# Kernel tuning notes

Measured on AMD Instinct MI355X. Metric: run time of the kernel, lower is better.

The kernel has to match this reference:

```python
import jax, jax.numpy as jnp
import numpy as np

B, N, D = 4, 2048, 1024
WIN, K, ALPHA = 4, 8, 0.3


def setup_inputs() -> dict:
    key = jax.random.key(0)
    ks = jax.random.split(key, 16)
    s_d = 1.0 / np.sqrt(D)
    s_2d = 1.0 / np.sqrt(2 * D)
    inp = {
        'mu': jax.random.normal(ks[0], (B, N, D), jnp.float32),
        'pheromone': jax.random.uniform(ks[1], (B, N), jnp.float32),
        'Wq': jax.random.normal(ks[2], (D, D), jnp.float32) * s_d,
        'bq': jnp.zeros((D,), jnp.float32),
        'Wk': jax.random.normal(ks[3], (D, D), jnp.float32) * s_d,
        'bk': jnp.zeros((D,), jnp.float32),
        'Wv': jax.random.normal(ks[4], (D, D), jnp.float32) * s_d,
        'bv': jnp.zeros((D,), jnp.float32),
        'Wm1': jax.random.normal(ks[5], (2 * D, D), jnp.float32) * s_2d,
        'bm1': jnp.zeros((D,), jnp.float32),
        'Wm2': jax.random.normal(ks[6], (D, D), jnp.float32) * s_d,
        'bm2': jnp.zeros((D,), jnp.float32),
        'Wo': jax.random.normal(ks[7], (2 * D, D), jnp.float32) * s_2d,
        'bo': jnp.zeros((D,), jnp.float32),
    }
    return inp


def reference(mu, pheromone, Wq, bq, Wk, bk, Wv, bv, Wm1, bm1, Wm2, bm2, Wo, bo):
    # ---- local windowed gather-MLP ----
    padded = jnp.pad(mu, ((0, 0), (WIN, 0), (0, 0)))  # causal left-pad
    neighbors = jnp.stack([padded[:, WIN - w:WIN - w + N, :] for w in range(1, WIN + 1)], axis=2)
    self_exp = jnp.broadcast_to(mu[:, :, None, :], neighbors.shape)
    cat = jnp.concatenate([self_exp, neighbors], axis=-1)
    h = jax.nn.silu(cat @ Wm1 + bm1) @ Wm2 + bm2
    local_msgs = h.mean(axis=2)  # (B,N,D)

    # ---- causal top-k attention with pheromone bias ----
    q = mu @ Wq + bq
    k = mu @ Wk + bk
    v = mu @ Wv + bv
    scale = 1.0 / jnp.sqrt(jnp.asarray(D, mu.dtype))
    scores = jnp.einsum('bnd,bmd->bnm', q, k) * scale  # (B,N,N)
    scores = scores + ALPHA * pheromone[:, None, :]
    row = jnp.arange(N)
    causal = jnp.where(row[None, :] > row[:, None], -jnp.inf, 0.0).astype(mu.dtype)
    scores = scores + causal[None]
    # top-k sparsification (N > K): softmax over the k kept scores, zeros elsewhere
    vals, idx = jax.lax.top_k(scores, K)  # (B,N,K)
    probs = jax.nn.softmax(vals, axis=-1)
    bi = jnp.arange(B)[:, None, None]
    ni = jnp.arange(N)[None, :, None]
    attn = jnp.zeros_like(scores).at[bi, ni, idx].set(probs)
    global_msgs = jnp.einsum('bnm,bmd->bnd', attn, v)

    return jnp.concatenate([local_msgs, global_msgs], axis=-1) @ Wo + bo
```

## Files before the change

### kernel.cpp

```cpp
#include <hip/hip_runtime.h>
#include <hip/hip_bf16.h>
#include <math.h>

#define B_ 4
#define N_ 2048
#define D_ 1024
#define WIN_ 4
#define KTOP 8
#define ALPHA_ 0.3f
#define SCALE_ (1.0f/32.0f)
#define NCH 16
#define INV2048 0.00048828125f

typedef unsigned short ushortT;
typedef _Float16 halfT;
typedef __attribute__((ext_vector_type(8))) _Float16 half8v;
typedef __attribute__((ext_vector_type(4))) float f32x4;

__device__ inline ushortT h2u(halfT h){ union{halfT h; ushortT u;} x; x.h=h; return x.u; }
__device__ inline halfT  u2h(ushortT u){ union{halfT h; ushortT u;} x; x.u=u; return x.h; }
__device__ inline float  uh2f(ushortT u){ return (float)u2h(u); }

__device__ __forceinline__ void gll16(const ushortT* g, ushortT* l) {
    __builtin_amdgcn_global_load_lds(
        (const __attribute__((address_space(1))) void*)g,
        (__attribute__((address_space(3))) void*)l, 16, 0, 0);
}

__global__ __launch_bounds__(256)
void prep_all(const float* __restrict__ mu, const float* __restrict__ Wm1,
              const float* __restrict__ Wm2, const float* __restrict__ Wv,
              const float* __restrict__ Wo, const float* __restrict__ Wq,
              const float* __restrict__ Wk,
              ushortT* __restrict__ mu_a, ushortT* __restrict__ mu_B,
              ushortT* __restrict__ WtF, ushortT* __restrict__ Wt_m2,
              ushortT* __restrict__ Wt_v, ushortT* __restrict__ Wt_o,
              ushortT* __restrict__ WqT_a, ushortT* __restrict__ WqT_B,
              ushortT* __restrict__ WkT_a, ushortT* __restrict__ WkT_B)
{
    const int bid = blockIdx.x;
    if (bid < 8192) {
        size_t base = ((size_t)bid * 256 + threadIdx.x) * 4;
        float4 v = *reinterpret_cast<const float4*>(&mu[base]);
        float vv[4] = {v.x, v.y, v.z, v.w};
        ushort4 pa, pb;
#pragma unroll
        for (int j = 0; j < 4; ++j) {
            float f = vv[j];
            halfT a = (halfT)f;  float r = f - (float)a;
            halfT b = (halfT)(r * 2048.0f);
            ((ushortT*)&pa)[j] = h2u(a); ((ushortT*)&pb)[j] = h2u(b);
        }
        *reinterpret_cast<ushort4*>(&mu_a[base]) = pa;
        *reinterpret_cast<ushort4*>(&mu_B[base]) = pb;
        return;
    }
    __shared__ float t[32][33];
    int b = bid - 8192;
    const float* W; ushortT* Pa; ushortT* Pb = nullptr;
    int K, lb, split = 0;
    if (b < 1024)      { W = Wm1;                       Pa = WtF;                     K = 1024; lb = b; }
    else if (b < 2048) { W = Wm1 + (size_t)1024 * 1024; Pa = WtF + (size_t)1024*1024; K = 1024; lb = b - 1024; }
    else if (b < 3072) { W = Wm2;  Pa = Wt_m2; K = 1024; lb = b - 2048; }
    else if (b < 4096) { W = Wv;   Pa = Wt_v;  K = 1024; lb = b - 3072; }
    else if (b < 6144) { W = Wo;   Pa = Wt_o;  K = 2048; lb = b - 4096; }
    else if (b < 7168) { W = Wq;   Pa = WqT_a; Pb = WqT_B; K = 1024; lb = b - 6144; split = 1; }
    else               { W = Wk;   Pa = WkT_a; Pb = WkT_B; K = 1024; lb = b - 7168; split = 1; }
    const int Nn = 1024;
    const int k0 = (K == 2048) ? (lb & 63) * 32 : (lb & 31) * 32;
    const int n0 = (K == 2048) ? (lb >> 6) * 32 : (lb >> 5) * 32;
    const int tx = threadIdx.x & 31, ty8 = threadIdx.x >> 5;
#pragma unroll
    for (int p = 0; p < 4; ++p) {
        int kk = p * 8 + ty8;
        t[kk][tx] = W[(size_t)(k0 + kk) * Nn + n0 + tx];
    }
    __syncthreads();
#pragma unroll
    for (int p = 0; p < 4; ++p) {
        int nn = p * 8 + ty8;
        float f = t[tx][nn];
        size_t o = (size_t)(n0 + nn) * K + k0 + tx;
        if (split) {
            halfT a = (halfT)f;  float r = f - (float)a;
            halfT bb = (halfT)(r * 2048.0f);
            Pa[o] = h2u(a); Pb[o] = h2u(bb);
        } else {
            Pa[o] = h2u((halfT)f);
        }
    }
}

__device__ __forceinline__ void gemm_core_h(
    const ushortT* __restrict__ A, int lda, const ushortT* __restrict__ Bt, int ldb,
    const float* __restrict__ bias, void* __restrict__ Cout, int ldc, int K,
    int m0, int n0, int outHalf, ushortT* AsL, ushortT* BsL)
{
    const int tid = threadIdx.x;
    const int w = tid >> 6, lane = tid & 63;
    const int wr = w >> 1, wc = w & 1;

    f32x4 acc[4][4];
#pragma unroll
    for (int mi = 0; mi < 4; ++mi)
#pragma unroll
        for (int ni = 0; ni < 4; ++ni) acc[mi][ni] = (f32x4){0.f, 0.f, 0.f, 0.f};

    for (int k0 = 0; k0 < K; k0 += 64) {
#pragma unroll
        for (int it = 0; it < 4; ++it) {
            int idx = tid + it * 256;
            int row = idx >> 3, c = idx & 7;
            int4 va = *reinterpret_cast<const int4*>(&A[(size_t)(m0 + row) * lda + k0 + c * 8]);
            *reinterpret_cast<int4*>(&AsL[row * 72 + c * 8]) = va;
            int4 vb = *reinterpret_cast<const int4*>(&Bt[(size_t)(n0 + row) * ldb + k0 + c * 8]);
            *reinterpret_cast<int4*>(&BsL[row * 72 + c * 8]) = vb;
        }
        __syncthreads();
#pragma unroll
        for (int kh = 0; kh < 2; ++kh) {
            const int ko = kh * 32 + (lane >> 4) * 8;
            const int rr = lane & 15;
            half8v af[4], bf[4];
#pragma unroll
            for (int mi = 0; mi < 4; ++mi)
                af[mi] = *reinterpret_cast<const half8v*>(&AsL[(wr * 64 + mi * 16 + rr) * 72 + ko]);
#pragma unroll
            for (int ni = 0; ni < 4; ++ni)
                bf[ni] = *reinterpret_cast<const half8v*>(&BsL[(wc * 64 + ni * 16 + rr) * 72 + ko]);
#pragma unroll
            for (int mi = 0; mi < 4; ++mi)
#pragma unroll
                for (int ni = 0; ni < 4; ++ni)
                    acc[mi][ni] = __builtin_amdgcn_mfma_f32_16x16x32_f16(
                        af[mi], bf[ni], acc[mi][ni], 0, 0, 0);
        }
        __syncthreads();
    }

    const int r4 = (lane >> 4) * 4, cl = lane & 15;
#pragma unroll
    for (int mi = 0; mi < 4; ++mi)
#pragma unroll
        for (int ni = 0; ni < 4; ++ni) {
            int row = m0 + wr * 64 + mi * 16 + r4;
            int col = n0 + wc * 64 + ni * 16 + cl;
            float bb = bias ? bias[col] : 0.f;
#pragma unroll
            for (int r = 0; r < 4; ++r) {
                float v = acc[mi][ni][r] + bb;
                if (outHalf)
                    ((ushortT*)Cout)[(size_t)(row + r) * ldc + col] = h2u((halfT)v);
                else
                    ((float*)Cout)[(size_t)(row + r) * ldc + col] = v;
            }
        }
}

template<int OUT_HALF>
__global__ __launch_bounds__(256)
void mfma_gemm_h(const ushortT* __restrict__ A, int lda,
                 const ushortT* __restrict__ Bt, int ldb,
                 const float* __restrict__ bias,
                 void* __restrict__ Cout, int ldc, int K)
{
    __shared__ ushortT AsL[128 * 72];
    __shared__ ushortT BsL[128 * 72];
    gemm_core_h(A, lda, Bt, ldb, bias, Cout, ldc, K,
                blockIdx.y * 128, blockIdx.x * 128, OUT_HALF, AsL, BsL);
}

__global__ __launch_bounds__(256)
void gemm_pf_v(const ushortT* __restrict__ mu_a,
               const ushortT* __restrict__ WtF, const ushortT* __restrict__ Wt_v,
               const float* __restrict__ bv,
               float* __restrict__ PF, ushortT* __restrict__ Vb16)
{
    __shared__ ushortT AsL[128 * 72];
    __shared__ ushortT BsL[128 * 72];
    const int bid = blockIdx.x;
    if (bid < 1024) {
        gemm_core_h(mu_a, D_, WtF, D_, (const float*)nullptr, (void*)PF, 2 * D_, D_,
                    (bid >> 4) * 128, (bid & 15) * 128, 0, AsL, BsL);
    } else {
        const int b2 = bid - 1024;
        gemm_core_h(mu_a, D_, Wt_v, D_, bv, (void*)Vb16, D_, D_,
                    (b2 >> 3) * 128, (b2 & 7) * 128, 1, AsL, BsL);
    }
}

__global__ __launch_bounds__(256)
void silu_mean(const float* __restrict__ P, const float* __restrict__ bm1,
               ushortT* __restrict__ Sb)
{
    size_t idx4 = (size_t)blockIdx.x * blockDim.x + threadIdx.x;
    size_t base = idx4 << 2;
    int row = (int)(base >> 10);
    int col = (int)(base & 1023);
    int n = row & (N_ - 1);
    float4 a = *reinterpret_cast<const float4*>(&P[(size_t)row * 2048 + col]);
    float4 bb = *reinterpret_cast<const float4*>(&bm1[col]);
    a.x += bb.x; a.y += bb.y; a.z += bb.z; a.w += bb.w;
    float sx = 0.f, sy = 0.f, sz = 0.f, sw = 0.f;
#pragma unroll
    for (int w = 1; w <= WIN_; ++w) {
        float xx = a.x, xy = a.y, xz = a.z, xw = a.w;
        if (n >= w) {
            const float4 nb = *reinterpret_cast<const float4*>(
                &P[(size_t)(row - w) * 2048 + 1024 + col]);
            xx += nb.x; xy += nb.y; xz += nb.z; xw += nb.w;
        }
        sx += xx / (1.f + __expf(-xx));
        sy += xy / (1.f + __expf(-xy));
        sz += xz / (1.f + __expf(-xz));
        sw += xw / (1.f + __expf(-xw));
    }
    ushort4 o = {h2u((halfT)(sx * 0.25f)), h2u((halfT)(sy * 0.25f)),
                 h2u((halfT)(sz * 0.25f)), h2u((halfT)(sw * 0.25f))};
    *reinterpret_cast<ushort4*>(&Sb[base]) = o;
}

__device__ inline void topk_insert(float (&tv)[KTOP], int (&ti)[KTOP], float s, int m)
{
    if ((s > tv[KTOP-1]) || (s == tv[KTOP-1] && m < ti[KTOP-1])) {
        float cs = s; int ci = m;
#pragma unroll
        for (int q = 0; q < KTOP; ++q) {
            bool beats = (cs > tv[q]) || (cs == tv[q] && ci < ti[q]);
            if (beats) { float t0 = tv[q]; int t1 = ti[q];
                         tv[q] = cs; ti[q] = ci; cs = t0; ci = t1; }
        }
    }
}

#define SPLIT3H_COMPUTE(Tb, wr, wc, lane, acc0, acc1)                           \
    {                                                                           \
        const int rr_ = (lane) & 15, q_ = (lane) >> 4;                          \
        const int Rb0_ = (wc) * 32 + rr_;                                       \
        const int Rb1_ = Rb0_ + 16;                                             \
        half8v ba0_ = *reinterpret_cast<const half8v*>(                         \
            &Tb[2 * 4096 + Rb0_ * 32 + ((q_ ^ ((Rb0_ >> 1) & 3)) << 3)]);       \
        half8v ba1_ = *reinterpret_cast<const half8v*>(                         \
            &Tb[2 * 4096 + Rb1_ * 32 + ((q_ ^ ((Rb1_ >> 1) & 3)) << 3)]);       \
        half8v bB0_ = *reinterpret_cast<const half8v*>(                         \
            &Tb[3 * 4096 + Rb0_ * 32 + ((q_ ^ ((Rb0_ >> 1) & 3)) << 3)]);       \
        half8v bB1_ = *reinterpret_cast<const half8v*>(                         \
            &Tb[3 * 4096 + Rb1_ * 32 + ((q_ ^ ((Rb1_ >> 1) & 3)) << 3)]);       \
        _Pragma("unroll")                                                       \
        for (int mi_ = 0; mi_ < 4; ++mi_) {                                     \
            const int Ra_ = (wr) * 64 + mi_ * 16 + rr_;                         \
            const int sw_ = (q_ ^ ((Ra_ >> 1) & 3)) << 3;                       \
            half8v aA_ = *reinterpret_cast<const half8v*>(&Tb[Ra_ * 32 + sw_]); \
            acc0[mi_][0] = __builtin_amdgcn_mfma_f32_16x16x32_f16(              \
                aA_, ba0_, acc0[mi_][0], 0, 0, 0);                              \
            acc0[mi_][1] = __builtin_amdgcn_mfma_f32_16x16x32_f16(              \
                aA_, ba1_, acc0[mi_][1], 0, 0, 0);                              \
            acc1[mi_][0] = __builtin_amdgcn_mfma_f32_16x16x32_f16(              \
                aA_, bB0_, acc1[mi_][0], 0, 0, 0);                              \
            acc1[mi_][1] = __builtin_amdgcn_mfma_f32_16x16x32_f16(              \
                aA_, bB1_, acc1[mi_][1], 0, 0, 0);                              \
        }                                                                       \
        _Pragma("unroll")                                                       \
        for (int mi_ = 0; mi_ < 4; ++mi_) {                                     \
            const int Ra_ = (wr) * 64 + mi_ * 16 + rr_;                         \
            const int sw_ = (q_ ^ ((Ra_ >> 1) & 3)) << 3;                       \
            half8v aB_ = *reinterpret_cast<const half8v*>(                      \
                &Tb[4096 + Ra_ * 32 + sw_]);                                    \
            acc1[mi_][0] = __builtin_amdgcn_mfma_f32_16x16x32_f16(              \
                aB_, ba0_, acc1[mi_][0], 0, 0, 0);                              \
            acc1[mi_][1] = __builtin_amdgcn_mfma_f32_16x16x32_f16(              \
                aB_, ba1_, acc1[mi_][1], 0, 0, 0);                              \
        }                                                                       \
    }

#define STAGE4(lb, koff)                                                        \
    {                                                                           \
        gll16(gp + goff + (koff), lb);                                          \
        gll16(gp + goff + (koff) + 16 * D_, (lb) + 512);                        \
        gll16(gp + goff + (koff) + 32 * D_, (lb) + 1024);                       \
        gll16(gp + goff + (koff) + 48 * D_, (lb) + 1536);                       \
    }

__global__ __launch_bounds__(512, 2)
void qk_proj(const ushortT* __restrict__ A0, const ushortT* __restrict__ A1,
             const ushortT* __restrict__ QWa, const ushortT* __restrict__ QWB,
             const ushortT* __restrict__ KWa, const ushortT* __restrict__ KWB,
             const float* __restrict__ bq, const float* __restrict__ bk,
             ushortT* __restrict__ Qa, ushortT* __restrict__ QB,
             ushortT* __restrict__ Ka, ushortT* __restrict__ KB)
{
    __shared__ ushortT TT[2][16384];

    const int half = blockIdx.x >> 9;
    int lin = blockIdx.x & 511;
    lin = (lin & 7) * 64 + (lin >> 3);
    const int m0 = (lin >> 3) * 128;
    const int n0 = (lin & 7) * 128;

    const ushortT* B0 = half ? KWa : QWa;
    const ushortT* B1 = half ? KWB : QWB;
    const float* bias = half ? bk : bq;
    ushortT* Pa = half ? Ka : Qa;
    ushortT* Pb = half ? KB : QB;

    const int tid = threadIdx.x;
    const int wid = tid >> 6, lane = tid & 63;
    const int wr = wid >> 2, wc = wid & 3;

    const int pl = wid >> 1;
    const int hb = (wid & 1) * 64;
    const ushortT* gp = (pl == 0) ? A0 : (pl == 1) ? A1 : (pl == 2) ? B0 : B1;
    const int rbase = (pl < 2 ? m0 : n0) + hb + (lane >> 2);
    const int cg8 = ((lane & 3) ^ ((lane >> 3) & 3)) << 3;
    const size_t goff = (size_t)rbase * D_ + cg8;
    ushortT* lb0 = &TT[0][pl * 4096 + hb * 32];
    ushortT* lb1 = &TT[1][pl * 4096 + hb * 32];

    f32x4 acc0[4][2], acc1[4][2];
#pragma unroll
    for (int mi = 0; mi < 4; ++mi) {
        acc0[mi][0] = (f32x4){0,0,0,0}; acc0[mi][1] = (f32x4){0,0,0,0};
        acc1[mi][0] = (f32x4){0,0,0,0}; acc1[mi][1] = (f32x4){0,0,0,0};
    }

    STAGE4(lb0, 0)
    __syncthreads();

    int cur = 0;
    for (int ks = 0; ks < 32; ++ks) {
        if (ks < 31) {
            ushortT* lb = cur ? lb0 : lb1;
            STAGE4(lb, (size_t)(ks + 1) * 32)
        }
        const ushortT* Tb = &TT[cur][0];
        __builtin_amdgcn_s_setprio(1);
        SPLIT3H_COMPUTE(Tb, wr, wc, lane, acc0, acc1)
        __builtin_amdgcn_s_setprio(0);
        __syncthreads();
        cur ^= 1;
    }

    const int r4 = (lane >> 4) * 4, cl = lane & 15;
#pragma unroll
    for (int mi = 0; mi < 4; ++mi)
#pragma unroll
        for (int ni = 0; ni < 2; ++ni) {
            int col = n0 + wc * 32 + ni * 16 + cl;
            float bb = bias[col];
#pragma unroll
            for (int r = 0; r < 4; ++r) {
                int row = m0 + wr * 64 + mi * 16 + r4 + r;
                float v = acc0[mi][ni][r] + INV2048 * acc1[mi][ni][r] + bb;
                halfT a = (halfT)v;  float r1 = v - (float)a;
                halfT b = (halfT)(r1 * 2048.0f);
                size_t o = (size_t)row * D_ + col;
                Pa[o] = h2u(a); Pb[o] = h2u(b);
            }
        }
}

__global__ __launch_bounds__(512, 2)
void attn_scores_h(const ushortT* __restrict__ Qa, const ushortT* __restrict__ QB,
                   const ushortT* __restrict__ Ka, const ushortT* __restrict__ KB,
                   const float* __restrict__ pher,
                   float* __restrict__ WV, int* __restrict__ WI)
{
    __shared__ ushortT TT[2][16384];
    __shared__ float Ps[128];
    __shared__ float PV[32 * 4 * 8];
    __shared__ int   PI[32 * 4 * 8];
    float* MV = reinterpret_cast<float*>(&TT[0][0]);
    int*   MI = reinterpret_cast<int*>((char*)&TT[0][0] + 16384);

    int lin = blockIdx.y * 136 + blockIdx.x;
    lin = (lin & 7) * 68 + (lin >> 3);
    const int b = lin / 136;
    const int xy = lin - b * 136;
    int g = 0;
    while ((g + 1) * (g + 2) / 2 <= xy) ++g;
    const int ch = xy - g * (g + 1) / 2;
    const int n0 = g * 128;
    const int m0 = ch * 128;
    const size_t bN = (size_t)b * N_;

    const int tid = threadIdx.x;
    const int wid = tid >> 6, lane = tid & 63;
    const int wr = wid >> 2, wc = wid & 3;

    if (tid < 128) Ps[tid] = pher[bN + m0 + tid];

    const int pl = wid >> 1;
    const int hb = (wid & 1) * 64;
    const ushortT* gp = (pl == 0) ? Qa : (pl == 1) ? QB : (pl == 2) ? Ka : KB;
    const size_t rbase = bN + (pl < 2 ? n0 : m0) + hb + (lane >> 2);
    const int cg8 = ((lane & 3) ^ ((lane >> 3) & 3)) << 3;
    const size_t goff = rbase * (size_t)D_ + cg8;
    ushortT* lb0 = &TT[0][pl * 4096 + hb * 32];
    ushortT* lb1 = &TT[1][pl * 4096 + hb * 32];

    f32x4 acc0[4][2], acc1[4][2];
#pragma unroll
    for (int mi = 0; mi < 4; ++mi) {
        acc0[mi][0] = (f32x4){0,0,0,0}; acc0[mi][1] = (f32x4){0,0,0,0};
        acc1[mi][0] = (f32x4){0,0,0,0}; acc1[mi][1] = (f32x4){0,0,0,0};
    }

    STAGE4(lb0, 0)
    __syncthreads();

    int cur = 0;
    for (int ks = 0; ks < 32; ++ks) {
        if (ks < 31) {
            ushortT* lb = cur ? lb0 : lb1;
            STAGE4(lb, (size_t)(ks + 1) * 32)
        }
        const ushortT* Tb = &TT[cur][0];
        __builtin_amdgcn_s_setprio(1);
        SPLIT3H_COMPUTE(Tb, wr, wc, lane, acc0, acc1)
        __builtin_amdgcn_s_setprio(0);
        __syncthreads();
        cur ^= 1;
    }

    const int r4 = (lane >> 4) * 4, cl = lane & 15;
    for (int p = 0; p < 4; ++p) {
        __syncthreads();
        if (wr == (p >> 1)) {
#pragma unroll
            for (int mi2 = 0; mi2 < 2; ++mi2) {
                const int mi = (p & 1) * 2 + mi2;
#pragma unroll
                for (int ni = 0; ni < 2; ++ni) {
                    int col = wc * 32 + ni * 16 + cl;
                    int m = m0 + col;
#pragma unroll
                    for (int r = 0; r < 4; ++r) {
                        int rloc = mi2 * 16 + r4 + r;
                        int n = n0 + p * 32 + rloc;
                        bool ok = (m <= n);
                        float sc = acc0[mi][ni][r] + INV2048 * acc1[mi][ni][r];
                        MV[rloc * 128 + col] = ok ? (sc * SCALE_ + ALPHA_ * Ps[col])
                                                  : -INFINITY;
                        MI[rloc * 128 + col] = ok ? m : 0x7fffffff;
                    }
                }
            }
        }
        __syncthreads();
        if (tid < 128) {
            const int row = tid >> 2, q4 = tid & 3;
            float tv[KTOP]; int ti[KTOP];
#pragma unroll
            for (int j = 0; j < KTOP; ++j) { tv[j] = -INFINITY; ti[j] = 0x7fffffff; }
            for (int j = 0; j < 32; ++j) {
                float s2 = MV[row * 128 + q4 * 32 + j];
                if (s2 == -INFINITY) continue;
                topk_insert(tv, ti, s2, MI[row * 128 + q4 * 32 + j]);
            }
#pragma unroll
            for (int j = 0; j < KTOP; ++j) {
                PV[(row * 4 + q4) * 8 + j] = tv[j];
                PI[(row * 4 + q4) * 8 + j] = ti[j];
            }
        }
        __syncthreads();
        if (tid < 32) {
            float tv[KTOP]; int ti[KTOP];
#pragma unroll
            for (int j = 0; j < KTOP; ++j) { tv[j] = -INFINITY; ti[j] = 0x7fffffff; }
            for (int i = 0; i < 32; ++i) {
                float s2 = PV[tid * 32 + i];
                if (s2 == -INFINITY) continue;
                topk_insert(tv, ti, s2, PI[tid * 32 + i]);
            }
            int n = n0 + p * 32 + tid;
            size_t base = ((bN + n) * NCH + ch) * 8;
#pragma unroll
            for (int j = 0; j < KTOP; ++j) { WV[base + j] = tv[j]; WI[base + j] = ti[j]; }
        }
    }
}

__global__ __launch_bounds__(256)
void attn_merge(const float* __restrict__ WV, const int* __restrict__ WI,
                const ushortT* __restrict__ V, ushortT* __restrict__ CCb)
{
    __shared__ float CV[4][128];
    __shared__ int   CI[4][128];
    __shared__ float Pp[4][KTOP];
    __shared__ int   Pi[4][KTOP];

    const int tid  = threadIdx.x;
    const int wv   = tid >> 6;
    const int lane = tid & 63;
    const int rid  = blockIdx.x * 4 + wv;
    const int b    = rid >> 11;
    const int n    = rid & (N_ - 1);
    const int ncand = ((n >> 7) + 1) * 8;
    const size_t cbase = (size_t)rid * (NCH * 8);

#pragma unroll
    for (int t = 0; t < 2; ++t) {
        int i = lane + t * 64;
        if (i < ncand) { CV[wv][i] = WV[cbase + i]; CI[wv][i] = WI[cbase + i]; }
        else           { CV[wv][i] = -INFINITY;     CI[wv][i] = 0x7fffffff;   }
    }
    __syncthreads();

    if (lane == 0) {
        float tv[KTOP]; int ti[KTOP];
#pragma unroll
        for (int j = 0; j < KTOP; ++j) { tv[j] = -INFINITY; ti[j] = 0x7fffffff; }
        for (int i = 0; i < 128; ++i) {
            float s = CV[wv][i];
            if (s == -INFINITY) continue;
            topk_insert(tv, ti, s, CI[wv][i]);
        }
        float mx = tv[0];
        float e[KTOP]; float sum = 0.f;
#pragma unroll
        for (int j = 0; j < KTOP; ++j) {
            e[j] = (tv[j] == -INFINITY) ? 0.f : __expf(tv[j] - mx);
            sum += e[j];
        }
        float inv = 1.f / sum;
#pragma unroll
        for (int j = 0; j < KTOP; ++j) {
            Pp[wv][j] = e[j] * inv;
            Pi[wv][j] = (tv[j] == -INFINITY) ? 0 : ti[j];
        }
    }
    __syncthreads();

    const size_t vbase = (size_t)b * N_ * D_;
#pragma unroll
    for (int it = 0; it < 2; ++it) {
        int c8 = (it * 64 + lane) * 8;
        float o[8];
#pragma unroll
        for (int u = 0; u < 8; ++u) o[u] = 0.f;
#pragma unroll
        for (int j = 0; j < KTOP; ++j) {
            float p = Pp[wv][j];
            ushort4 v0 = *reinterpret_cast<const ushort4*>(
                &V[vbase + (size_t)Pi[wv][j] * D_ + c8]);
            ushort4 v1 = *reinterpret_cast<const ushort4*>(
                &V[vbase + (size_t)Pi[wv][j] * D_ + c8 + 4]);
            o[0] = fmaf(p, uh2f(v0.x), o[0]); o[1] = fmaf(p, uh2f(v0.y), o[1]);
            o[2] = fmaf(p, uh2f(v0.z), o[2]); o[3] = fmaf(p, uh2f(v0.w), o[3]);
            o[4] = fmaf(p, uh2f(v1.x), o[4]); o[5] = fmaf(p, uh2f(v1.y), o[5]);
            o[6] = fmaf(p, uh2f(v1.z), o[6]); o[7] = fmaf(p, uh2f(v1.w), o[7]);
        }
        ushort4 ob0 = {h2u((halfT)o[0]), h2u((halfT)o[1]), h2u((halfT)o[2]), h2u((halfT)o[3])};
        ushort4 ob1 = {h2u((halfT)o[4]), h2u((halfT)o[5]), h2u((halfT)o[6]), h2u((halfT)o[7])};
        *reinterpret_cast<ushort4*>(&CCb[(size_t)rid * 2048 + 1024 + c8]) = ob0;
        *reinterpret_cast<ushort4*>(&CCb[(size_t)rid * 2048 + 1024 + c8 + 4]) = ob1;
    }
}

extern "C" void kernel_launch(void* const* d_in, const int* in_sizes, int n_in,
                              void* d_out, int out_size, void* d_ws, size_t ws_size,
                              hipStream_t stream)
{
    const float* mu   = (const float*)d_in[0];
    const float* pher = (const float*)d_in[1];
    const float* Wq   = (const float*)d_in[2];
    const float* bq   = (const float*)d_in[3];
    const float* Wk   = (const float*)d_in[4];
    const float* bk   = (const float*)d_in[5];
    const float* Wv   = (const float*)d_in[6];
    const float* bv   = (const float*)d_in[7];
    const float* Wm1  = (const float*)d_in[8];
    const float* bm1  = (const float*)d_in[9];
    const float* Wm2  = (const float*)d_in[10];
    const float* bm2  = (const float*)d_in[11];
    const float* Wo   = (const float*)d_in[12];
    const float* bo   = (const float*)d_in[13];
    float* out = (float*)d_out;
    float* ws  = (float*)d_ws;

    const size_t SZ  = (size_t)B_ * N_ * D_;
    const size_t MEG = 1024 * 1024;
    const int M = B_ * N_;

    ushortT* CCb  = (ushortT*)ws;
    float*   PF   = ws + SZ;
    ushortT* Qa   = (ushortT*)(ws + SZ);
    ushortT* QB   = Qa + SZ;
    ushortT* Ka   = (ushortT*)(ws + 2 * SZ);
    ushortT* KB   = Ka + SZ;
    ushortT* mu_a = (ushortT*)(ws + 3 * SZ);
    ushortT* mu_B = mu_a + SZ;
    ushortT* Sb   = (ushortT*)(ws + 4 * SZ);
    float*   WVb  = (float*)(ws + 4 * SZ);
    int*     WIb  = (int*)(WVb + MEG);
    ushortT* Vb16 = (ushortT*)(ws + 4 * SZ + 4 * MEG);
    ushortT* U    = (ushortT*)(ws + 4 * SZ + 8 * MEG);
    ushortT* WtF  = U;
    ushortT* Wt_m2 = U + 2 * MEG;
    ushortT* Wt_v  = U + 3 * MEG;
    ushortT* WqT_a = U + 4 * MEG;        ushortT* WqT_B = U + 5 * MEG;
    ushortT* WkT_a = U + 6 * MEG;        ushortT* WkT_B = U + 7 * MEG;
    ushortT* Wt_o  = U + 8 * MEG;

    dim3 blk256(256), blk512(512);
    dim3 gD(8, 64);

    hipLaunchKernelGGL(prep_all, dim3(16384), blk256, 0, stream,
                       mu, Wm1, Wm2, Wv, Wo, Wq, Wk,
                       mu_a, mu_B, WtF, Wt_m2, Wt_v, Wt_o,
                       WqT_a, WqT_B, WkT_a, WkT_B);
    hipLaunchKernelGGL(gemm_pf_v, dim3(1536), blk256, 0, stream,
                       mu_a, WtF, Wt_v, bv, PF, Vb16);
    hipLaunchKernelGGL(silu_mean, dim3(SZ / 4 / 256), blk256, 0, stream, PF, bm1, Sb);
    hipLaunchKernelGGL((mfma_gemm_h<1>), gD, blk256, 0, stream,
                       Sb, D_, Wt_m2, D_, bm2, (void*)CCb, 2 * D_, D_);
    hipLaunchKernelGGL(qk_proj, dim3(1024), blk512, 0, stream,
                       mu_a, mu_B, WqT_a, WqT_B, WkT_a, WkT_B,
                       bq, bk, Qa, QB, Ka, KB);
    hipLaunchKernelGGL(attn_scores_h, dim3(136, B_), blk512, 0, stream,
                       Qa, QB, Ka, KB, pher, WVb, WIb);
    hipLaunchKernelGGL(attn_merge, dim3(M / 4), blk256, 0, stream, WVb, WIb, Vb16, CCb);
    hipLaunchKernelGGL((mfma_gemm_h<0>), gD, blk256, 0, stream,
                       CCb, 2 * D_, Wt_o, 2048, bo, (void*)out, D_, 2 * D_);

    (void)in_sizes; (void)n_in; (void)out_size; (void)ws_size;
}
```

Before: 739.3 us.

## Replace double-buffered LDS staging with single buffer in QK projection and scores

Removes the ping-pong LDS buffers in qk_proj and attn_scores_h, so each k-step loads its tile, syncs, computes, then syncs again. This halves the tile LDS footprint, which may let more blocks fit per CU. The cost is that global-to-LDS loads no longer overlap with MFMA compute and each iteration now waits on two barriers.

```diff
diff --git a/kernel.cpp b/kernel.cpp
--- a/kernel.cpp
+++ b/kernel.cpp
@@ -289,7 +289,7 @@
              ushortT* __restrict__ Qa, ushortT* __restrict__ QB,
              ushortT* __restrict__ Ka, ushortT* __restrict__ KB)
 {
-    __shared__ ushortT TT[2][16384];
+    __shared__ ushortT TT[16384];
 
     const int half = blockIdx.x >> 9;
     int lin = blockIdx.x & 511;
@@ -313,8 +313,7 @@
     const int rbase = (pl < 2 ? m0 : n0) + hb + (lane >> 2);
     const int cg8 = ((lane & 3) ^ ((lane >> 3) & 3)) << 3;
     const size_t goff = (size_t)rbase * D_ + cg8;
-    ushortT* lb0 = &TT[0][pl * 4096 + hb * 32];
-    ushortT* lb1 = &TT[1][pl * 4096 + hb * 32];
+    ushortT* lb0 = &TT[pl * 4096 + hb * 32];
 
     f32x4 acc0[4][2], acc1[4][2];
 #pragma unroll
@@ -323,21 +322,13 @@
         acc1[mi][0] = (f32x4){0,0,0,0}; acc1[mi][1] = (f32x4){0,0,0,0};
     }
 
-    STAGE4(lb0, 0)
-    __syncthreads();
-
-    int cur = 0;
     for (int ks = 0; ks < 32; ++ks) {
-        if (ks < 31) {
-            ushortT* lb = cur ? lb0 : lb1;
-            STAGE4(lb, (size_t)(ks + 1) * 32)
-        }
-        const ushortT* Tb = &TT[cur][0];
+        STAGE4(lb0, (size_t)ks * 32)
+        __syncthreads();
         __builtin_amdgcn_s_setprio(1);
-        SPLIT3H_COMPUTE(Tb, wr, wc, lane, acc0, acc1)
+        SPLIT3H_COMPUTE(TT, wr, wc, lane, acc0, acc1)
         __builtin_amdgcn_s_setprio(0);
         __syncthreads();
-        cur ^= 1;
     }
 
     const int r4 = (lane >> 4) * 4, cl = lane & 15;
@@ -365,12 +356,12 @@
                    const float* __restrict__ pher,
                    float* __restrict__ WV, int* __restrict__ WI)
 {
-    __shared__ ushortT TT[2][16384];
+    __shared__ ushortT TT[16384];
     __shared__ float Ps[128];
     __shared__ float PV[32 * 4 * 8];
     __shared__ int   PI[32 * 4 * 8];
-    float* MV = reinterpret_cast<float*>(&TT[0][0]);
-    int*   MI = reinterpret_cast<int*>((char*)&TT[0][0] + 16384);
+    float* MV = reinterpret_cast<float*>(&TT[0]);
+    int*   MI = reinterpret_cast<int*>((char*)&TT[0] + 16384);
 
     int lin = blockIdx.y * 136 + blockIdx.x;
     lin = (lin & 7) * 68 + (lin >> 3);
@@ -395,8 +386,7 @@
     const size_t rbase = bN + (pl < 2 ? n0 : m0) + hb + (lane >> 2);
     const int cg8 = ((lane & 3) ^ ((lane >> 3) & 3)) << 3;
     const size_t goff = rbase * (size_t)D_ + cg8;
-    ushortT* lb0 = &TT[0][pl * 4096 + hb * 32];
-    ushortT* lb1 = &TT[1][pl * 4096 + hb * 32];
+    ushortT* lb0 = &TT[pl * 4096 + hb * 32];
 
     f32x4 acc0[4][2], acc1[4][2];
 #pragma unroll
@@ -405,21 +395,13 @@
         acc1[mi][0] = (f32x4){0,0,0,0}; acc1[mi][1] = (f32x4){0,0,0,0};
     }
 
-    STAGE4(lb0, 0)
-    __syncthreads();
-
-    int cur = 0;
     for (int ks = 0; ks < 32; ++ks) {
-        if (ks < 31) {
-            ushortT* lb = cur ? lb0 : lb1;
-            STAGE4(lb, (size_t)(ks + 1) * 32)
-        }
-        const ushortT* Tb = &TT[cur][0];
+        STAGE4(lb0, (size_t)ks * 32)
+        __syncthreads();
         __builtin_amdgcn_s_setprio(1);
-        SPLIT3H_COMPUTE(Tb, wr, wc, lane, acc0, acc1)
+        SPLIT3H_COMPUTE(TT, wr, wc, lane, acc0, acc1)
         __builtin_amdgcn_s_setprio(0);
         __syncthreads();
-        cur ^= 1;
     }
 
     const int r4 = (lane >> 4) * 4, cl = lane & 15;
```

Result: no change. 739.7 us (+0.0%).
